# Optimization experiments

Hardware: AMD Instinct MI355X
Metric: run time of the kernel (lower is better)

## Reference

```python
import jax, jax.numpy as jnp
import numpy as np

B, S, D, F, E = 4, 4096, 1024, 2048, 8


def setup_inputs() -> dict:
    key = jax.random.key(0)
    ks = jax.random.split(key, 8)
    x = jax.random.normal(ks[0], (B, S, D), dtype=jnp.float32)
    # router (nn.Linear(d_model, num_experts))
    Wr = jax.random.normal(ks[1], (D, E), dtype=jnp.float32) * 0.02
    br = jnp.zeros((E,), dtype=jnp.float32)
    # stacked per-expert MLP params: Linear(D,F) -> GELU -> Linear(F,D)
    W1 = jax.random.normal(ks[2], (E, D, F), dtype=jnp.float32) * (1.0 / np.sqrt(D))
    b1 = jnp.zeros((E, F), dtype=jnp.float32)
    W2 = jax.random.normal(ks[3], (E, F, D), dtype=jnp.float32) * (1.0 / np.sqrt(F))
    b2 = jnp.zeros((E, D), dtype=jnp.float32)
    return {"x": x, "Wr": Wr, "br": br, "W1": W1, "b1": b1, "W2": W2, "b2": b2}


def reference(x, Wr, br, W1, b1, W2, b2):
    # router: softmax over experts, top-1 selection
    logits = jnp.einsum("bsd,de->bse", x, Wr) + br          # [B,S,E]
    probs = jax.nn.softmax(logits, axis=-1)
    expert_weights = jnp.max(probs, axis=-1)                  # [B,S]
    expert_indices = jnp.argmax(probs, axis=-1)               # [B,S]

    num_experts = W1.shape[0]
    out = jnp.zeros_like(x)
    # loop over the small fixed set of experts (structurally distinct weights)
    for e in range(num_experts):
        h = jax.nn.gelu(jnp.einsum("bsd,df->bsf", x, W1[e]) + b1[e], approximate=False)
        y = jnp.einsum("bsf,fd->bsd", h, W2[e]) + b2[e]
        out = jnp.where((expert_indices == e)[..., None], y, out)

    return out * expert_weights[..., None]
```

## Files before the change

kernel.cpp:

```cpp
#include <hip/hip_runtime.h>
#include <hip/hip_bf16.h>


typedef __attribute__((ext_vector_type(8))) short short8;
typedef __attribute__((ext_vector_type(4))) float f32x4;

struct __align__(8) us4 { unsigned short x, y, z, w; };

__device__ __forceinline__ void gload16(const void* g, void* l) {
  __builtin_amdgcn_global_load_lds(
      (const __attribute__((address_space(1))) unsigned int*)g,
      (__attribute__((address_space(3))) unsigned int*)l, 16, 0, 0);
}

__device__ __forceinline__ unsigned short f2b(float f) {
  union { float f; unsigned u; } v; v.f = f;
  unsigned r = v.u + 0x7FFFu + ((v.u >> 16) & 1u);
  return (unsigned short)(r >> 16);
}

__global__ __launch_bounds__(256) void router_logits(
    const float* __restrict__ x, const float* __restrict__ Wr,
    const float* __restrict__ br, float* __restrict__ wts,
    int* __restrict__ eidx, unsigned short* __restrict__ xb)
{
  const int lane = threadIdx.x & 63;
  const int wid  = threadIdx.x >> 6;
  const int t = blockIdx.x * 4 + wid;

  const float4* x4 = (const float4*)(x + (size_t)t * 1024);
  float acc[8];
#pragma unroll
  for (int e = 0; e < 8; ++e) acc[e] = 0.f;
#pragma unroll
  for (int i = 0; i < 4; ++i) {
    float4 v = x4[lane + 64 * i];
    const int d = (lane + 64 * i) * 4;
    const float* wr = Wr + (size_t)d * 8;
    float xs[4] = {v.x, v.y, v.z, v.w};
    us4 o;
    o.x = f2b(v.x); o.y = f2b(v.y); o.z = f2b(v.z); o.w = f2b(v.w);
    *(us4*)(xb + (size_t)t * 1024 + (size_t)(lane + 64 * i) * 4) = o;
#pragma unroll
    for (int j = 0; j < 4; ++j) {
      float4 w0 = *(const float4*)(wr + j * 8);
      float4 w1 = *(const float4*)(wr + j * 8 + 4);
      acc[0] += xs[j] * w0.x; acc[1] += xs[j] * w0.y;
      acc[2] += xs[j] * w0.z; acc[3] += xs[j] * w0.w;
      acc[4] += xs[j] * w1.x; acc[5] += xs[j] * w1.y;
      acc[6] += xs[j] * w1.z; acc[7] += xs[j] * w1.w;
    }
  }
#pragma unroll
  for (int e = 0; e < 8; ++e) {
    float v = acc[e];
#pragma unroll
    for (int m = 32; m; m >>= 1) v += __shfl_xor(v, m, 64);
    acc[e] = v;
  }
  if (lane == 0) {
    float lg[8];
#pragma unroll
    for (int e = 0; e < 8; ++e) lg[e] = acc[e] + br[e];
    float mx = lg[0]; int bi = 0;
#pragma unroll
    for (int e = 1; e < 8; ++e) if (lg[e] > mx) { mx = lg[e]; bi = e; }
    float s = 0.f;
#pragma unroll
    for (int e = 0; e < 8; ++e) s += expf(lg[e] - mx);
    wts[t]  = 1.0f / s;
    eidx[t] = bi;
  }
}

__global__ __launch_bounds__(256) void bucketize(
    const int* __restrict__ eidx, int* __restrict__ cnt, int* __restrict__ list)
{
  __shared__ int lcnt[8], base[8];
  const int tid = threadIdx.x;
  if (tid < 8) lcnt[tid] = 0;
  __syncthreads();
  const int t = blockIdx.x * 256 + tid;
  const int e = eidx[t];
  const int lpos = atomicAdd(&lcnt[e], 1);
  __syncthreads();
  if (tid < 8) base[tid] = atomicAdd(&cnt[tid], lcnt[tid]);
  __syncthreads();
  list[e * 16384 + base[e] + lpos] = t;
}

__global__ __launch_bounds__(256) void transpose_cvt(
    const float* __restrict__ W, unsigned short* __restrict__ Wt, int K, int N)
{
  __shared__ float tl[64][65];
  const int e = blockIdx.z;
  const float* Wp = W + (size_t)e * K * N;
  unsigned short* Wtp = Wt + (size_t)e * K * N;
  const int k0 = blockIdx.y * 64, n0 = blockIdx.x * 64;
  const int r = threadIdx.x >> 4, c4 = (threadIdx.x & 15) * 4;
#pragma unroll
  for (int i = 0; i < 4; ++i) {
    float4 v = *(const float4*)(Wp + (size_t)(k0 + r + i * 16) * N + n0 + c4);
    tl[r + i * 16][c4 + 0] = v.x; tl[r + i * 16][c4 + 1] = v.y;
    tl[r + i * 16][c4 + 2] = v.z; tl[r + i * 16][c4 + 3] = v.w;
  }
  __syncthreads();
#pragma unroll
  for (int i = 0; i < 4; ++i) {
    const int n = r + i * 16;
    us4 o;
    o.x = f2b(tl[c4 + 0][n]); o.y = f2b(tl[c4 + 1][n]);
    o.z = f2b(tl[c4 + 2][n]); o.w = f2b(tl[c4 + 3][n]);
    *(us4*)(Wtp + (size_t)(n0 + n) * K + k0 + c4) = o;
  }
}

template <int K, int N, int EPI, int LOGNB>
__global__ __launch_bounds__(512, 2) void gemm_moe8(
    const unsigned short* __restrict__ A,
    const unsigned short* __restrict__ Bt,
    const float* __restrict__ bias,
    const int* __restrict__ cnt, const int* __restrict__ list,
    const float* __restrict__ wts, void* __restrict__ outp)
{
  constexpr int NT = K / 32;
  constexpr int NB = 1 << LOGNB;
  extern __shared__ char lds[];
  int*   tok_s = (int*)(lds + 65536);
  float* wt_s  = (float*)(lds + 66560);

  const int q = gridDim.x >> 3;
  const int p = ((int)blockIdx.x & 7) * q + ((int)blockIdx.x >> 3);
  int e = -1, pre = 0, cnte = 0, loc = p;
#pragma unroll
  for (int i = 0; i < 8; ++i) {
    const int c = cnt[i];
    const int bl = ((c + 255) >> 8) << LOGNB;
    if (e < 0) {
      if (loc < bl) { e = i; cnte = c; }
      else { loc -= bl; pre += c; }
    }
  }
  if (e < 0) return;
  const int row0 = (loc >> LOGNB) << 8;
  const int n0   = (loc & (NB - 1)) << 8;

  const int tid = threadIdx.x;
  const int lane = tid & 63, wid = tid >> 6;
  const int wr = wid >> 2, wc = wid & 3;
  const int l15 = lane & 15;

  if (tid < 256) {
    const int s = row0 + tid;
    if (s < cnte) {
      const int t = list[e * 16384 + s];
      tok_s[tid] = t;
      wt_s[tid]  = (EPI == 2) ? wts[t] : 0.f;
    } else { tok_s[tid] = 0; wt_s[tid] = 0.f; }
  }
  __syncthreads();

  const int srow = tid >> 2;
  const int gch  = ((tid & 3) ^ ((srow >> 1) & 3)) * 8;
  const unsigned short* aG0;
  const unsigned short* aG1;
  if (EPI == 1) {
    aG0 = A + (size_t)tok_s[srow] * K + gch;
    aG1 = A + (size_t)tok_s[128 + srow] * K + gch;
  } else {
    aG0 = A + (size_t)min(pre + row0 + srow, 16383) * K + gch;
    aG1 = A + (size_t)min(pre + row0 + 128 + srow, 16383) * K + gch;
  }
  const unsigned short* bG0 = Bt + ((size_t)e * N + n0 + srow) * K + gch;
  const unsigned short* bG1 = Bt + ((size_t)e * N + n0 + 128 + srow) * K + gch;

  const int xo = (((lane >> 4) ^ ((l15 >> 1) & 3)) << 4);
  const char* aB = lds + wr * 8192 + l15 * 64 + xo;
  const char* bB = lds + 32768 + wc * 4096 + l15 * 64 + xo;

  f32x4 acc[8][4];
#pragma unroll
  for (int m = 0; m < 8; ++m)
#pragma unroll
    for (int n = 0; n < 4; ++n) acc[m][n] = (f32x4){0.f, 0.f, 0.f, 0.f};

#define STG_A(S, T) do { \
    char* d_ = lds + (S) * 16384 + (wid << 10); \
    gload16(aG0 + (size_t)(T) * 32, d_); \
    gload16(aG1 + (size_t)(T) * 32, d_ + 8192); } while (0)
#define STG_B(S, T) do { \
    char* d_ = lds + 32768 + (S) * 16384 + (wid << 10); \
    gload16(bG0 + (size_t)(T) * 32, d_); \
    gload16(bG1 + (size_t)(T) * 32, d_ + 8192); } while (0)

  STG_A(0, 0); STG_B(0, 0);
  asm volatile("s_waitcnt vmcnt(0)" ::: "memory");
  __builtin_amdgcn_s_barrier();

  short8 aF[8], bF[4];
#pragma unroll 1
  for (int T = 0; T < NT; ++T) {
    const int buf = T & 1;
    const int Ts  = (T + 1 < NT) ? T + 1 : NT - 1;
    STG_A(buf ^ 1, Ts);
    STG_B(buf ^ 1, Ts);
    const char* aT = aB + buf * 16384;
    const char* bT = bB + buf * 16384;
#pragma unroll
    for (int m = 0; m < 8; ++m) aF[m] = *(const short8*)(aT + m * 1024);
#pragma unroll
    for (int n = 0; n < 4; ++n) bF[n] = *(const short8*)(bT + n * 1024);
    asm volatile("s_waitcnt lgkmcnt(0)" ::: "memory");
    __builtin_amdgcn_sched_barrier(0);
    __builtin_amdgcn_s_setprio(1);
#pragma unroll
    for (int m = 0; m < 8; ++m)
#pragma unroll
      for (int n = 0; n < 4; ++n)
        acc[m][n] = __builtin_amdgcn_mfma_f32_16x16x32_bf16(
            aF[m], bF[n], acc[m][n], 0, 0, 0);
    __builtin_amdgcn_s_setprio(0);
    __builtin_amdgcn_sched_barrier(0);
    asm volatile("s_waitcnt vmcnt(0)" ::: "memory");
    __builtin_amdgcn_s_barrier();
  }
#undef STG_A
#undef STG_B

  const int cRow0 = wr * 128 + ((lane >> 4) << 2);
  const int cColB = n0 + wc * 64 + l15;
  float bv[4];
#pragma unroll
  for (int nf = 0; nf < 4; ++nf) bv[nf] = bias[e * N + cColB + nf * 16];

  if (EPI == 1) {
    unsigned short* H = (unsigned short*)outp;
#pragma unroll
    for (int m = 0; m < 8; ++m)
#pragma unroll
      for (int r = 0; r < 4; ++r) {
        const int sl = cRow0 + m * 16 + r;
        if (row0 + sl < cnte) {
          const size_t rp = (size_t)(pre + row0 + sl) * N + cColB;
#pragma unroll
          for (int nf = 0; nf < 4; ++nf) {
            float v = acc[m][nf][r] + bv[nf];
            float u = 1.5957691216f * v * (1.0f + 0.044715f * v * v);
            float ex = __expf(u);
            float th = 1.0f - 2.0f / (ex + 1.0f);
            v = 0.5f * v * (1.0f + th);
            H[rp + nf * 16] = f2b(v);
          }
        }
      }
  } else {
    float* O = (float*)outp;
#pragma unroll
    for (int m = 0; m < 8; ++m)
#pragma unroll
      for (int r = 0; r < 4; ++r) {
        const int sl = cRow0 + m * 16 + r;
        if (row0 + sl < cnte) {
          const size_t rp = (size_t)tok_s[sl] * N + cColB;
          const float w = wt_s[sl];
#pragma unroll
          for (int nf = 0; nf < 4; ++nf)
            O[rp + nf * 16] = (acc[m][nf][r] + bv[nf]) * w;
        }
      }
  }
}

extern "C" void kernel_launch(void* const* d_in, const int* in_sizes, int n_in,
                              void* d_out, int out_size, void* d_ws, size_t ws_size,
                              hipStream_t stream) {
  const float* x  = (const float*)d_in[0];
  const float* Wr = (const float*)d_in[1];
  const float* br = (const float*)d_in[2];
  const float* W1 = (const float*)d_in[3];
  const float* b1 = (const float*)d_in[4];
  const float* W2 = (const float*)d_in[5];
  const float* b2 = (const float*)d_in[6];

  char* ws = (char*)d_ws;
  int*   cnt  = (int*)ws;
  float* wts  = (float*)(ws + 256);
  int*   eidx = (int*)(ws + 256 + 64 * 1024);
  int*   list = (int*)(ws + 256 + 128 * 1024);
  unsigned short* xb  = (unsigned short*)(ws + 1024 * 1024);
  unsigned short* w1t = xb  + (size_t)16384 * 1024;
  unsigned short* w2t = w1t + (size_t)8 * 2048 * 1024;
  unsigned short* h   = w2t + (size_t)8 * 1024 * 2048;

  constexpr int LDS_BYTES = 67584;
  hipFuncSetAttribute((const void*)gemm_moe8<1024, 2048, 1, 3>,
                      hipFuncAttributeMaxDynamicSharedMemorySize, LDS_BYTES);
  hipFuncSetAttribute((const void*)gemm_moe8<2048, 1024, 2, 2>,
                      hipFuncAttributeMaxDynamicSharedMemorySize, LDS_BYTES);

  hipMemsetAsync(cnt, 0, 32, stream);
  router_logits<<<dim3(4096), 256, 0, stream>>>(x, Wr, br, wts, eidx, xb);
  bucketize<<<dim3(64), 256, 0, stream>>>(eidx, cnt, list);
  transpose_cvt<<<dim3(32, 16, 8), 256, 0, stream>>>(W1, w1t, 1024, 2048);
  transpose_cvt<<<dim3(16, 32, 8), 256, 0, stream>>>(W2, w2t, 2048, 1024);
  gemm_moe8<1024, 2048, 1, 3><<<dim3(71 * 8), 512, LDS_BYTES, stream>>>(
      xb, w1t, b1, cnt, list, wts, (void*)h);
  gemm_moe8<2048, 1024, 2, 2><<<dim3(71 * 4), 512, LDS_BYTES, stream>>>(
      h, w2t, b2, cnt, list, wts, d_out);
}
```

Before: 366.5 us.

## Double K-tile depth and split MoE GEMM main loop into four interleaved phases

Raises the K step per iteration from 32 to 64, which doubles the LDS tiles to 128 KB with a new XOR swizzle and loader mapping. The main loop is split into four MFMA quadrant phases separated by barriers, with the next tile's A and B global-to-LDS loads issued between phases. The aim is to overlap loads with compute and halve the per-iteration barrier and wait overhead. The cost is that 133 KB of LDS likely limits each CU to one 512-thread block instead of the two the launch bounds request, and it adds many more barriers. The second GEMM's grid also grows slightly.

```diff
diff --git a/kernel.cpp b/kernel.cpp
--- a/kernel.cpp
+++ b/kernel.cpp
@@ -123,11 +123,11 @@
     const int* __restrict__ cnt, const int* __restrict__ list,
     const float* __restrict__ wts, void* __restrict__ outp)
 {
-  constexpr int NT = K / 32;
+  constexpr int NT = K / 64;
   constexpr int NB = 1 << LOGNB;
   extern __shared__ char lds[];
-  int*   tok_s = (int*)(lds + 65536);
-  float* wt_s  = (float*)(lds + 66560);
+  int*   tok_s = (int*)(lds + 131072);
+  float* wt_s  = (float*)(lds + 132096);
 
   const int q = gridDim.x >> 3;
   const int p = ((int)blockIdx.x & 7) * q + ((int)blockIdx.x >> 3);
@@ -148,7 +148,7 @@
   const int tid = threadIdx.x;
   const int lane = tid & 63, wid = tid >> 6;
   const int wr = wid >> 2, wc = wid & 3;
-  const int l15 = lane & 15;
+  const int l15 = lane & 15, hi = lane >> 4;
 
   if (tid < 256) {
     const int s = row0 + tid;
@@ -160,23 +160,24 @@
   }
   __syncthreads();
 
-  const int srow = tid >> 2;
-  const int gch  = ((tid & 3) ^ ((srow >> 1) & 3)) * 8;
-  const unsigned short* aG0;
-  const unsigned short* aG1;
-  if (EPI == 1) {
-    aG0 = A + (size_t)tok_s[srow] * K + gch;
-    aG1 = A + (size_t)tok_s[128 + srow] * K + gch;
-  } else {
-    aG0 = A + (size_t)min(pre + row0 + srow, 16383) * K + gch;
-    aG1 = A + (size_t)min(pre + row0 + 128 + srow, 16383) * K + gch;
-  }
-  const unsigned short* bG0 = Bt + ((size_t)e * N + n0 + srow) * K + gch;
-  const unsigned short* bG1 = Bt + ((size_t)e * N + n0 + 128 + srow) * K + gch;
-
-  const int xo = (((lane >> 4) ^ ((l15 >> 1) & 3)) << 4);
-  const char* aB = lds + wr * 8192 + l15 * 64 + xo;
-  const char* bB = lds + 32768 + wc * 4096 + l15 * 64 + xo;
+  const int r8 = lane >> 3;
+  const int ch = (lane & 7) ^ r8;
+  const unsigned short* aP[4];
+  const unsigned short* bP[4];
+#pragma unroll
+  for (int k2 = 0; k2 < 4; ++k2) {
+    const int row = wid * 8 + r8 + k2 * 64;
+    if (EPI == 1) aP[k2] = A + (size_t)tok_s[row] * K + ch * 8;
+    else          aP[k2] = A + (size_t)min(pre + row0 + row, 16383) * K + ch * 8;
+    bP[k2] = Bt + ((size_t)e * N + n0 + row) * K + ch * 8;
+  }
+
+  const int sl0 = ((hi ^ (l15 & 7)) << 4);
+  const int sl1 = (((4 + hi) ^ (l15 & 7)) << 4);
+  const char* aR0 = lds + (size_t)(wr * 128 + l15) * 128 + sl0;
+  const char* aR1 = lds + (size_t)(wr * 128 + l15) * 128 + sl1;
+  const char* bR0 = lds + 65536 + (size_t)(wc * 64 + l15) * 128 + sl0;
+  const char* bR1 = lds + 65536 + (size_t)(wc * 64 + l15) * 128 + sl1;
 
   f32x4 acc[8][4];
 #pragma unroll
@@ -184,50 +185,106 @@
 #pragma unroll
     for (int n = 0; n < 4; ++n) acc[m][n] = (f32x4){0.f, 0.f, 0.f, 0.f};
 
-#define STG_A(S, T) do { \
-    char* d_ = lds + (S) * 16384 + (wid << 10); \
-    gload16(aG0 + (size_t)(T) * 32, d_); \
-    gload16(aG1 + (size_t)(T) * 32, d_ + 8192); } while (0)
-#define STG_B(S, T) do { \
-    char* d_ = lds + 32768 + (S) * 16384 + (wid << 10); \
-    gload16(bG0 + (size_t)(T) * 32, d_); \
-    gload16(bG1 + (size_t)(T) * 32, d_ + 8192); } while (0)
+#define STG_A(BUF, T) do { _Pragma("unroll") \
+    for (int k2 = 0; k2 < 4; ++k2) \
+      gload16(aP[k2] + (size_t)(T) * 64, lds + (BUF) * 32768 + wid * 1024 + k2 * 8192); \
+  } while (0)
+#define STG_B(BUF, T) do { _Pragma("unroll") \
+    for (int k2 = 0; k2 < 4; ++k2) \
+      gload16(bP[k2] + (size_t)(T) * 64, lds + 65536 + (BUF) * 32768 + wid * 1024 + k2 * 8192); \
+  } while (0)
+#define BARF() do { __builtin_amdgcn_s_barrier(); asm volatile("" ::: "memory"); } while (0)
 
   STG_A(0, 0); STG_B(0, 0);
   asm volatile("s_waitcnt vmcnt(0)" ::: "memory");
-  __builtin_amdgcn_s_barrier();
-
-  short8 aF[8], bF[4];
+  BARF();
+
+  short8 aF[8], bA[4], bB[4];
 #pragma unroll 1
   for (int T = 0; T < NT; ++T) {
-    const int buf = T & 1;
-    const int Ts  = (T + 1 < NT) ? T + 1 : NT - 1;
-    STG_A(buf ^ 1, Ts);
-    STG_B(buf ^ 1, Ts);
-    const char* aT = aB + buf * 16384;
-    const char* bT = bB + buf * 16384;
-#pragma unroll
-    for (int m = 0; m < 8; ++m) aF[m] = *(const short8*)(aT + m * 1024);
-#pragma unroll
-    for (int n = 0; n < 4; ++n) bF[n] = *(const short8*)(bT + n * 1024);
-    asm volatile("s_waitcnt lgkmcnt(0)" ::: "memory");
-    __builtin_amdgcn_sched_barrier(0);
+    const int buf = T & 1, bufn = buf ^ 1;
+    const int Ts = (T + 1 < NT) ? T + 1 : NT - 1;
+    const char* a0 = aR0 + buf * 32768;
+    const char* a1 = aR1 + buf * 32768;
+    const char* b0 = bR0 + buf * 32768;
+    const char* b1 = bR1 + buf * 32768;
+
+#pragma unroll
+    for (int m = 0; m < 4; ++m) {
+      aF[2 * m]     = *(const short8*)(a0 + m * 2048);
+      aF[2 * m + 1] = *(const short8*)(a1 + m * 2048);
+    }
+#pragma unroll
+    for (int n = 0; n < 2; ++n) {
+      bA[2 * n]     = *(const short8*)(b0 + n * 2048);
+      bA[2 * n + 1] = *(const short8*)(b1 + n * 2048);
+    }
+    STG_A(bufn, Ts);
+    BARF();
     __builtin_amdgcn_s_setprio(1);
 #pragma unroll
-    for (int m = 0; m < 8; ++m)
-#pragma unroll
-      for (int n = 0; n < 4; ++n)
-        acc[m][n] = __builtin_amdgcn_mfma_f32_16x16x32_bf16(
-            aF[m], bF[n], acc[m][n], 0, 0, 0);
+    for (int m = 0; m < 4; ++m)
+#pragma unroll
+      for (int n = 0; n < 2; ++n) {
+        acc[m][n] = __builtin_amdgcn_mfma_f32_16x16x32_bf16(aF[2 * m], bA[2 * n], acc[m][n], 0, 0, 0);
+        acc[m][n] = __builtin_amdgcn_mfma_f32_16x16x32_bf16(aF[2 * m + 1], bA[2 * n + 1], acc[m][n], 0, 0, 0);
+      }
     __builtin_amdgcn_s_setprio(0);
-    __builtin_amdgcn_sched_barrier(0);
+    BARF();
+
+#pragma unroll
+    for (int n = 0; n < 2; ++n) {
+      bB[2 * n]     = *(const short8*)(b0 + (2 + n) * 2048);
+      bB[2 * n + 1] = *(const short8*)(b1 + (2 + n) * 2048);
+    }
+    STG_B(bufn, Ts);
+    BARF();
+    __builtin_amdgcn_s_setprio(1);
+#pragma unroll
+    for (int m = 0; m < 4; ++m)
+#pragma unroll
+      for (int n = 0; n < 2; ++n) {
+        acc[m][2 + n] = __builtin_amdgcn_mfma_f32_16x16x32_bf16(aF[2 * m], bB[2 * n], acc[m][2 + n], 0, 0, 0);
+        acc[m][2 + n] = __builtin_amdgcn_mfma_f32_16x16x32_bf16(aF[2 * m + 1], bB[2 * n + 1], acc[m][2 + n], 0, 0, 0);
+      }
+    __builtin_amdgcn_s_setprio(0);
+    BARF();
+
+#pragma unroll
+    for (int m = 0; m < 4; ++m) {
+      aF[2 * m]     = *(const short8*)(a0 + (4 + m) * 2048);
+      aF[2 * m + 1] = *(const short8*)(a1 + (4 + m) * 2048);
+    }
+    BARF();
+    __builtin_amdgcn_s_setprio(1);
+#pragma unroll
+    for (int m = 0; m < 4; ++m)
+#pragma unroll
+      for (int n = 0; n < 2; ++n) {
+        acc[4 + m][2 + n] = __builtin_amdgcn_mfma_f32_16x16x32_bf16(aF[2 * m], bB[2 * n], acc[4 + m][2 + n], 0, 0, 0);
+        acc[4 + m][2 + n] = __builtin_amdgcn_mfma_f32_16x16x32_bf16(aF[2 * m + 1], bB[2 * n + 1], acc[4 + m][2 + n], 0, 0, 0);
+      }
+    __builtin_amdgcn_s_setprio(0);
+    BARF();
+
     asm volatile("s_waitcnt vmcnt(0)" ::: "memory");
-    __builtin_amdgcn_s_barrier();
+    BARF();
+    __builtin_amdgcn_s_setprio(1);
+#pragma unroll
+    for (int m = 0; m < 4; ++m)
+#pragma unroll
+      for (int n = 0; n < 2; ++n) {
+        acc[4 + m][n] = __builtin_amdgcn_mfma_f32_16x16x32_bf16(aF[2 * m], bA[2 * n], acc[4 + m][n], 0, 0, 0);
+        acc[4 + m][n] = __builtin_amdgcn_mfma_f32_16x16x32_bf16(aF[2 * m + 1], bA[2 * n + 1], acc[4 + m][n], 0, 0, 0);
+      }
+    __builtin_amdgcn_s_setprio(0);
+    BARF();
   }
 #undef STG_A
 #undef STG_B
-
-  const int cRow0 = wr * 128 + ((lane >> 4) << 2);
+#undef BARF
+
+  const int cRow0 = wr * 128 + (hi << 2);
   const int cColB = n0 + wc * 64 + l15;
   float bv[4];
 #pragma unroll
@@ -292,7 +349,7 @@
   unsigned short* w2t = w1t + (size_t)8 * 2048 * 1024;
   unsigned short* h   = w2t + (size_t)8 * 1024 * 2048;
 
-  constexpr int LDS_BYTES = 67584;
+  constexpr int LDS_BYTES = 133120;
   hipFuncSetAttribute((const void*)gemm_moe8<1024, 2048, 1, 3>,
                       hipFuncAttributeMaxDynamicSharedMemorySize, LDS_BYTES);
   hipFuncSetAttribute((const void*)gemm_moe8<2048, 1024, 2, 2>,
@@ -305,6 +362,6 @@
   transpose_cvt<<<dim3(16, 32, 8), 256, 0, stream>>>(W2, w2t, 2048, 1024);
   gemm_moe8<1024, 2048, 1, 3><<<dim3(71 * 8), 512, LDS_BYTES, stream>>>(
       xb, w1t, b1, cnt, list, wts, (void*)h);
-  gemm_moe8<2048, 1024, 2, 2><<<dim3(71 * 4), 512, LDS_BYTES, stream>>>(
+  gemm_moe8<2048, 1024, 2, 2><<<dim3(72 * 4), 512, LDS_BYTES, stream>>>(
       h, w2t, b2, cnt, list, wts, d_out);
 }
```

Result: no change. 360.3 us (-1.7%).
